# Kernel optimization log

Measured on AMD Instinct MI355X. Metric: run time of the kernel, lower is better.

Reference implementation:

```python
import jax, jax.numpy as jnp
import numpy as np

P = 50000    # number of POIs (rows of HG_pu, size of square A)
U = 100000   # number of users (rows of HG_up)
NNZ = 1600000
D = 128      # emb_dim


def setup_inputs() -> dict:
    key = jax.random.key(0)
    ks = jax.random.split(key, 8)
    x = jax.random.normal(ks[0], (P, D), dtype=jnp.float32)
    e = jax.random.normal(ks[1], (P, D), dtype=jnp.float32)
    vals_up = jax.random.uniform(ks[2], (NNZ,), dtype=jnp.float32)
    vals_pu = jax.random.uniform(ks[3], (NNZ,), dtype=jnp.float32)
    rows_up = jax.random.randint(ks[4], (NNZ,), 0, U, dtype=jnp.int32)
    cols_up = jax.random.randint(ks[5], (NNZ,), 0, P, dtype=jnp.int32)
    rows_pu = jax.random.randint(ks[6], (NNZ,), 0, P, dtype=jnp.int32)
    cols_pu = jax.random.randint(ks[7], (NNZ,), 0, U, dtype=jnp.int32)
    return {"t": 0, "x": x, "e": e,
            "vals_up": vals_up, "vals_pu": vals_pu,
            "rows_up": rows_up, "cols_up": cols_up,
            "rows_pu": rows_pu, "cols_pu": cols_pu}


def _spmm(vals, rows, cols, dense, num_rows):
    # sparse [num_rows, *] @ dense -> [num_rows, D]
    gathered = vals[:, None] * dense[cols]          # [nnz, D]
    return jax.ops.segment_sum(gathered, rows, num_segments=num_rows)


def reference(t, x, e, vals_up, vals_pu, rows_up, cols_up, rows_pu, cols_pu):
    # A = HG_pu @ HG_up (never materialized);  out = (A - I) @ x + e
    y = _spmm(vals_up, rows_up, cols_up, x, U)      # HG_up @ x : [U, D]
    z = _spmm(vals_pu, rows_pu, cols_pu, y, P)      # HG_pu @ y : [P, D]
    return z - x + e                                # (A - I) x + e
```

## Files before the change

kernel.cpp:

```cpp
#include <hip/hip_runtime.h>

#define NP 50000
#define NU 100000
#define NNZ_C 1600000
#define NNZ2 (2 * NNZ_C)
#define DIM 128
#define NR_TOT (NU + NP)

#define RBSH 7
#define RB 128
#define NBK ((NR_TOT + RB - 1) / RB)
#define ITEMS 8192
#define IPT (ITEMS / 256)
#define NBLK ((NNZ2 + ITEMS - 1) / ITEMS)

__device__ inline unsigned pack_bf16x2(float a, float b) {
    unsigned ia = __float_as_uint(a), ib = __float_as_uint(b);
    ia = (ia + 0x7FFFu + ((ia >> 16) & 1u)) >> 16;
    ib = (ib + 0x7FFFu + ((ib >> 16) & 1u)) >> 16;
    return ia | (ib << 16);
}

__device__ inline float dec_val(unsigned p) {
    return __uint_as_float((p & 0x7FFFu) << 16);
}

__global__ void cvt_bf16_kernel(const float* __restrict__ x,
                                unsigned* __restrict__ xh, int nwords) {
    int i = blockIdx.x * blockDim.x + threadIdx.x;
    if (i >= nwords) return;
    float2 v = ((const float2*)x)[i];
    xh[i] = pack_bf16x2(v.x, v.y);
}


__global__ void p1_hist_kernel(const int* __restrict__ rows_up,
                               const int* __restrict__ rows_pu,
                               int* __restrict__ hist_all) {
    __shared__ int h[NBK];
    for (int k = threadIdx.x; k < NBK; k += 256) h[k] = 0;
    __syncthreads();
    int base = blockIdx.x * ITEMS;
    for (int k = 0; k < IPT; ++k) {
        int i = base + k * 256 + threadIdx.x;
        if (i >= NNZ2) break;
        int r = (i < NNZ_C) ? rows_up[i] : (NU + rows_pu[i - NNZ_C]);
        atomicAdd(&h[r >> RBSH], 1);
    }
    __syncthreads();
    for (int k = threadIdx.x; k < NBK; k += 256)
        hist_all[k * NBLK + blockIdx.x] = h[k];
}

__global__ void p1_scan_kernel(const int* __restrict__ hist_all,
                               int* __restrict__ base_all,
                               int* __restrict__ totals) {
    __shared__ int lds[512];
    int b = blockIdx.x;
    int v = (threadIdx.x < NBLK) ? hist_all[b * NBLK + threadIdx.x] : 0;
    lds[threadIdx.x] = v;
    __syncthreads();
    for (int off = 1; off < 512; off <<= 1) {
        int t = (threadIdx.x >= (unsigned)off) ? lds[threadIdx.x - off] : 0;
        __syncthreads();
        lds[threadIdx.x] += t;
        __syncthreads();
    }
    if (threadIdx.x < NBLK) base_all[b * NBLK + threadIdx.x] = lds[threadIdx.x] - v;
    if (threadIdx.x == 511) totals[b] = lds[511];
}

__global__ void bucket_base_scan_kernel(const int* __restrict__ totals,
                                        int* __restrict__ bbase) {
    __shared__ int lds[1024];
    __shared__ int carry;
    if (threadIdx.x == 0) carry = 0;
    __syncthreads();
    for (int start = 0; start < NBK; start += 1024) {
        int i = start + threadIdx.x;
        int v = (i < NBK) ? totals[i] : 0;
        lds[threadIdx.x] = v;
        __syncthreads();
        for (int off = 1; off < 1024; off <<= 1) {
            int t = (threadIdx.x >= (unsigned)off) ? lds[threadIdx.x - off] : 0;
            __syncthreads();
            lds[threadIdx.x] += t;
            __syncthreads();
        }
        if (i < NBK) bbase[i] = carry + lds[threadIdx.x] - v;
        int tot = lds[1023];
        __syncthreads();
        if (threadIdx.x == 0) carry += tot;
        __syncthreads();
    }
    if (threadIdx.x == 0) bbase[NBK] = carry;
}

__global__ void p1_scatter_kernel(const float* __restrict__ vals_up,
                                  const float* __restrict__ vals_pu,
                                  const int* __restrict__ rows_up,
                                  const int* __restrict__ rows_pu,
                                  const int* __restrict__ cols_up,
                                  const int* __restrict__ cols_pu,
                                  const int* __restrict__ base_all,
                                  const int* __restrict__ bbase,
                                  int2* __restrict__ staging) {
    __shared__ int off[NBK];
    for (int k = threadIdx.x; k < NBK; k += 256) off[k] = 0;
    __syncthreads();
    int base = blockIdx.x * ITEMS;
    for (int k = 0; k < IPT; ++k) {
        int i = base + k * 256 + threadIdx.x;
        if (i >= NNZ2) break;
        int r, c; float v;
        if (i < NNZ_C) { r = rows_up[i]; c = cols_up[i]; v = vals_up[i]; }
        else { int q = i - NNZ_C; r = NU + rows_pu[q]; c = cols_pu[q]; v = vals_pu[q]; }
        int b = r >> RBSH;
        int lp = atomicAdd(&off[b], 1);
        unsigned vb = __float_as_uint(v);
        unsigned vr = (vb + 0x7FFFu + ((vb >> 16) & 1u)) >> 16;
        int pos = bbase[b] + base_all[b * NBLK + blockIdx.x] + lp;
        staging[pos] = make_int2((int)(((unsigned)c << 15) | vr), r);
    }
}

__global__ void p2_finalize_kernel(const int2* __restrict__ staging,
                                   const int* __restrict__ bbase,
                                   unsigned* __restrict__ packed,
                                   int* __restrict__ row_beg,
                                   int* __restrict__ row_cnt) {
    __shared__ int cnt[RB];
    __shared__ int scn[RB];
    __shared__ int cur[RB];
    int b = blockIdx.x;
    int beg = bbase[b], end = bbase[b + 1];
    if (threadIdx.x < RB) cnt[threadIdx.x] = 0;
    __syncthreads();
    for (int i = beg + threadIdx.x; i < end; i += 256)
        atomicAdd(&cnt[staging[i].y & (RB - 1)], 1);
    __syncthreads();
    if (threadIdx.x < RB) scn[threadIdx.x] = cnt[threadIdx.x];
    __syncthreads();
    for (int off = 1; off < RB; off <<= 1) {
        int t = 0;
        if (threadIdx.x < RB && threadIdx.x >= (unsigned)off) t = scn[threadIdx.x - off];
        __syncthreads();
        if (threadIdx.x < RB) scn[threadIdx.x] += t;
        __syncthreads();
    }
    if (threadIdx.x < RB) {
        int excl = scn[threadIdx.x] - cnt[threadIdx.x];
        cur[threadIdx.x] = beg + excl;
        int rr = (b << RBSH) + threadIdx.x;
        if (rr < NR_TOT) { row_beg[rr] = beg + excl; row_cnt[rr] = cnt[threadIdx.x]; }
    }
    __syncthreads();
    for (int i = beg + threadIdx.x; i < end; i += 256) {
        int2 it = staging[i];
        int pos = atomicAdd(&cur[it.y & (RB - 1)], 1);
        packed[pos] = (unsigned)it.x;
    }
}


__device__ inline void gather_row(const unsigned* __restrict__ packed,
                                  const unsigned* __restrict__ src,
                                  int beg, int end, int lane, float2& acc) {
    for (int chunk = beg; chunk < end; chunk += 64) {
        int cn = min(64, end - chunk);
        unsigned pw = (chunk + lane < end) ? packed[chunk + lane] : 0;
        int j = 0;
        for (; j + 7 < cn; j += 8) {
            unsigned p0 = (unsigned)__shfl((int)pw, j);
            unsigned p1 = (unsigned)__shfl((int)pw, j + 1);
            unsigned p2 = (unsigned)__shfl((int)pw, j + 2);
            unsigned p3 = (unsigned)__shfl((int)pw, j + 3);
            unsigned p4 = (unsigned)__shfl((int)pw, j + 4);
            unsigned p5 = (unsigned)__shfl((int)pw, j + 5);
            unsigned p6 = (unsigned)__shfl((int)pw, j + 6);
            unsigned p7 = (unsigned)__shfl((int)pw, j + 7);
            unsigned u0 = src[(p0 >> 15) * 64 + lane];
            unsigned u1 = src[(p1 >> 15) * 64 + lane];
            unsigned u2 = src[(p2 >> 15) * 64 + lane];
            unsigned u3 = src[(p3 >> 15) * 64 + lane];
            unsigned u4 = src[(p4 >> 15) * 64 + lane];
            unsigned u5 = src[(p5 >> 15) * 64 + lane];
            unsigned u6 = src[(p6 >> 15) * 64 + lane];
            unsigned u7 = src[(p7 >> 15) * 64 + lane];
            acc.x += dec_val(p0) * __uint_as_float(u0 << 16);
            acc.y += dec_val(p0) * __uint_as_float(u0 & 0xFFFF0000u);
            acc.x += dec_val(p1) * __uint_as_float(u1 << 16);
            acc.y += dec_val(p1) * __uint_as_float(u1 & 0xFFFF0000u);
            acc.x += dec_val(p2) * __uint_as_float(u2 << 16);
            acc.y += dec_val(p2) * __uint_as_float(u2 & 0xFFFF0000u);
            acc.x += dec_val(p3) * __uint_as_float(u3 << 16);
            acc.y += dec_val(p3) * __uint_as_float(u3 & 0xFFFF0000u);
            acc.x += dec_val(p4) * __uint_as_float(u4 << 16);
            acc.y += dec_val(p4) * __uint_as_float(u4 & 0xFFFF0000u);
            acc.x += dec_val(p5) * __uint_as_float(u5 << 16);
            acc.y += dec_val(p5) * __uint_as_float(u5 & 0xFFFF0000u);
            acc.x += dec_val(p6) * __uint_as_float(u6 << 16);
            acc.y += dec_val(p6) * __uint_as_float(u6 & 0xFFFF0000u);
            acc.x += dec_val(p7) * __uint_as_float(u7 << 16);
            acc.y += dec_val(p7) * __uint_as_float(u7 & 0xFFFF0000u);
        }
        for (; j + 3 < cn; j += 4) {
            unsigned p0 = (unsigned)__shfl((int)pw, j);
            unsigned p1 = (unsigned)__shfl((int)pw, j + 1);
            unsigned p2 = (unsigned)__shfl((int)pw, j + 2);
            unsigned p3 = (unsigned)__shfl((int)pw, j + 3);
            unsigned u0 = src[(p0 >> 15) * 64 + lane];
            unsigned u1 = src[(p1 >> 15) * 64 + lane];
            unsigned u2 = src[(p2 >> 15) * 64 + lane];
            unsigned u3 = src[(p3 >> 15) * 64 + lane];
            acc.x += dec_val(p0) * __uint_as_float(u0 << 16);
            acc.y += dec_val(p0) * __uint_as_float(u0 & 0xFFFF0000u);
            acc.x += dec_val(p1) * __uint_as_float(u1 << 16);
            acc.y += dec_val(p1) * __uint_as_float(u1 & 0xFFFF0000u);
            acc.x += dec_val(p2) * __uint_as_float(u2 << 16);
            acc.y += dec_val(p2) * __uint_as_float(u2 & 0xFFFF0000u);
            acc.x += dec_val(p3) * __uint_as_float(u3 << 16);
            acc.y += dec_val(p3) * __uint_as_float(u3 & 0xFFFF0000u);
        }
        for (; j < cn; ++j) {
            unsigned p = (unsigned)__shfl((int)pw, j);
            unsigned u = src[(p >> 15) * 64 + lane];
            float v = dec_val(p);
            acc.x += v * __uint_as_float(u << 16);
            acc.y += v * __uint_as_float(u & 0xFFFF0000u);
        }
    }
}

__global__ void spmm_gather_kernel(const int* __restrict__ row_beg,
                                   const int* __restrict__ row_cnt,
                                   const unsigned* __restrict__ packed,
                                   const unsigned* __restrict__ src,
                                   unsigned* __restrict__ dst) {
    int r = blockIdx.x * 4 + (threadIdx.x >> 6);
    if (r >= NU) return;
    int lane = threadIdx.x & 63;
    int beg = row_beg[r], end = beg + row_cnt[r];
    float2 acc = make_float2(0.f, 0.f);
    gather_row(packed, src, beg, end, lane, acc);
    dst[r * 64 + lane] = pack_bf16x2(acc.x, acc.y);
}

__global__ void spmm_gather_fused_kernel(const int* __restrict__ row_beg,
                                         const int* __restrict__ row_cnt,
                                         const unsigned* __restrict__ packed,
                                         const unsigned* __restrict__ src,
                                         const float* __restrict__ x,
                                         const float* __restrict__ e,
                                         float* __restrict__ out) {
    int r = blockIdx.x * 4 + (threadIdx.x >> 6);
    if (r >= NP) return;
    int lane = threadIdx.x & 63;
    int beg = row_beg[NU + r], end = beg + row_cnt[NU + r];
    float2 acc = make_float2(0.f, 0.f);
    gather_row(packed, src, beg, end, lane, acc);
    float2 xv = ((const float2*)(x + (size_t)r * DIM))[lane];
    float2 ev = ((const float2*)(e + (size_t)r * DIM))[lane];
    float2 o;
    o.x = acc.x - xv.x + ev.x;
    o.y = acc.y - xv.y + ev.y;
    ((float2*)(out + (size_t)r * DIM))[lane] = o;
}

extern "C" void kernel_launch(void* const* d_in, const int* in_sizes, int n_in,
                              void* d_out, int out_size, void* d_ws, size_t ws_size,
                              hipStream_t stream) {
    const float* x       = (const float*)d_in[1];
    const float* e       = (const float*)d_in[2];
    const float* vals_up = (const float*)d_in[3];
    const float* vals_pu = (const float*)d_in[4];
    const int*   rows_up = (const int*)d_in[5];
    const int*   cols_up = (const int*)d_in[6];
    const int*   rows_pu = (const int*)d_in[7];
    const int*   cols_pu = (const int*)d_in[8];
    float* out = (float*)d_out;

    char* ws = (char*)d_ws;
    unsigned* yh     = (unsigned*)(ws);
    int2* staging    = (int2*)(ws);
    unsigned* xh     = (unsigned*)(ws + 25600000);
    unsigned* packed = (unsigned*)(ws + 38400000);
    int* hist_all    = (int*)(ws + 51200000);
    int* base_all    = (int*)(ws + 53033248);
    int* totals      = (int*)(ws + 54866496);
    int* bbase       = (int*)(ws + 54871184);
    int* row_beg     = (int*)(ws + 54875904);
    int* row_cnt     = (int*)(ws + 55475904);

    cvt_bf16_kernel<<<(NP * 64 + 255) / 256, 256, 0, stream>>>(x, xh, NP * 64);

    p1_hist_kernel<<<NBLK, 256, 0, stream>>>(rows_up, rows_pu, hist_all);
    p1_scan_kernel<<<NBK, 512, 0, stream>>>(hist_all, base_all, totals);
    bucket_base_scan_kernel<<<1, 1024, 0, stream>>>(totals, bbase);
    p1_scatter_kernel<<<NBLK, 256, 0, stream>>>(vals_up, vals_pu,
                                                rows_up, rows_pu,
                                                cols_up, cols_pu,
                                                base_all, bbase, staging);
    p2_finalize_kernel<<<NBK, 256, 0, stream>>>(staging, bbase, packed,
                                                row_beg, row_cnt);

    spmm_gather_kernel<<<(NU + 3) / 4, 256, 0, stream>>>(row_beg, row_cnt,
                                                         packed, xh, yh);

    spmm_gather_fused_kernel<<<(NP + 3) / 4, 256, 0, stream>>>(row_beg, row_cnt,
                                                               packed, yh,
                                                               x, e, out);
}
```

Measured before the change: 387.3 us.

## Locally sort scatter chunks in LDS and split staging into payload and row byte

The bucket scatter kernel now processes each block's items in chunks of 4096. It builds a per-chunk bucket histogram and scan in shared memory, reorders entries by bucket in LDS, and then writes them to global staging in contiguous runs, so the scattered global stores become more coalesced. Staging is also split into a 4-byte payload array and a 1-byte local-row array instead of an 8-byte int2, which cuts staging traffic in both the scatter and finalize kernels. The cost is extra shared memory, more barriers and scan work per chunk, and lower occupancy from the larger LDS footprint.

Result: faster. 349.0 us (-9.9%).

```diff
diff --git a/kernel.cpp b/kernel.cpp
--- a/kernel.cpp
+++ b/kernel.cpp
@@ -11,8 +11,9 @@
 #define RB 128
 #define NBK ((NR_TOT + RB - 1) / RB)
 #define ITEMS 8192
-#define IPT (ITEMS / 256)
 #define NBLK ((NNZ2 + ITEMS - 1) / ITEMS)
+#define CHUNK 4096
+#define CPT (CHUNK / 256)
 
 __device__ inline unsigned pack_bf16x2(float a, float b) {
     unsigned ia = __float_as_uint(a), ib = __float_as_uint(b);
@@ -41,7 +42,7 @@
     for (int k = threadIdx.x; k < NBK; k += 256) h[k] = 0;
     __syncthreads();
     int base = blockIdx.x * ITEMS;
-    for (int k = 0; k < IPT; ++k) {
+    for (int k = 0; k < ITEMS / 256; ++k) {
         int i = base + k * 256 + threadIdx.x;
         if (i >= NNZ2) break;
         int r = (i < NNZ_C) ? rows_up[i] : (NU + rows_pu[i - NNZ_C]);
@@ -104,27 +105,92 @@
                                   const int* __restrict__ cols_pu,
                                   const int* __restrict__ base_all,
                                   const int* __restrict__ bbase,
-                                  int2* __restrict__ staging) {
+                                  unsigned* __restrict__ stag_pay,
+                                  unsigned char* __restrict__ stag_row) {
+    __shared__ unsigned spay[CHUNK];
+    __shared__ unsigned char srow[CHUNK];
+    __shared__ int sdst[CHUNK];
+    __shared__ int h[NBK];
+    __shared__ int cbase[NBK];
     __shared__ int off[NBK];
-    for (int k = threadIdx.x; k < NBK; k += 256) off[k] = 0;
-    __syncthreads();
-    int base = blockIdx.x * ITEMS;
-    for (int k = 0; k < IPT; ++k) {
-        int i = base + k * 256 + threadIdx.x;
-        if (i >= NNZ2) break;
-        int r, c; float v;
-        if (i < NNZ_C) { r = rows_up[i]; c = cols_up[i]; v = vals_up[i]; }
-        else { int q = i - NNZ_C; r = NU + rows_pu[q]; c = cols_pu[q]; v = vals_pu[q]; }
-        int b = r >> RBSH;
-        int lp = atomicAdd(&off[b], 1);
-        unsigned vb = __float_as_uint(v);
-        unsigned vr = (vb + 0x7FFFu + ((vb >> 16) & 1u)) >> 16;
-        int pos = bbase[b] + base_all[b * NBLK + blockIdx.x] + lp;
-        staging[pos] = make_int2((int)(((unsigned)c << 15) | vr), r);
-    }
-}
-
-__global__ void p2_finalize_kernel(const int2* __restrict__ staging,
+    __shared__ int tsum[256];
+
+    int tid = threadIdx.x;
+    int blk = blockIdx.x;
+    for (int k = tid; k < NBK; k += 256)
+        cbase[k] = bbase[k] + base_all[k * NBLK + blk];
+    int base = blk * ITEMS;
+
+    for (int c = 0; c < ITEMS / CHUNK; ++c) {
+        int cbeg = base + c * CHUNK;
+        int cnt_items = NNZ2 - cbeg;
+        if (cnt_items <= 0) break;
+        if (cnt_items > CHUNK) cnt_items = CHUNK;
+
+        for (int k = tid; k < NBK; k += 256) { h[k] = 0; off[k] = 0; }
+        __syncthreads();
+
+        unsigned rpay[CPT];
+        int rrow[CPT];
+        for (int k = 0; k < CPT; ++k) {
+            int i = cbeg + k * 256 + tid;
+            if (i < NNZ2) {
+                int r, cc; float v;
+                if (i < NNZ_C) { r = rows_up[i]; cc = cols_up[i]; v = vals_up[i]; }
+                else { int q = i - NNZ_C; r = NU + rows_pu[q]; cc = cols_pu[q]; v = vals_pu[q]; }
+                unsigned vb = __float_as_uint(v);
+                unsigned vr = (vb + 0x7FFFu + ((vb >> 16) & 1u)) >> 16;
+                rpay[k] = ((unsigned)cc << 15) | vr;
+                rrow[k] = r;
+                atomicAdd(&h[r >> RBSH], 1);
+            } else {
+                rrow[k] = -1;
+            }
+        }
+        __syncthreads();
+
+        {
+            int s0 = tid * 5;
+            int s1 = s0 + 5; if (s1 > NBK) s1 = NBK; if (s0 > NBK) s0 = NBK;
+            int a = 0;
+            for (int s = s0; s < s1; ++s) a += h[s];
+            tsum[tid] = a;
+            __syncthreads();
+            for (int o = 1; o < 256; o <<= 1) {
+                int t2 = (tid >= o) ? tsum[tid - o] : 0;
+                __syncthreads();
+                tsum[tid] += t2;
+                __syncthreads();
+            }
+            int run = (tid == 0) ? 0 : tsum[tid - 1];
+            for (int s = s0; s < s1; ++s) { int cc2 = h[s]; h[s] = run; run += cc2; }
+        }
+        __syncthreads();
+
+        for (int k = 0; k < CPT; ++k) {
+            if (rrow[k] < 0) continue;
+            int b = rrow[k] >> RBSH;
+            int lp = atomicAdd(&off[b], 1);
+            int slot = h[b] + lp;
+            spay[slot] = rpay[k];
+            srow[slot] = (unsigned char)(rrow[k] & (RB - 1));
+            sdst[slot] = cbase[b] + lp;
+        }
+        __syncthreads();
+
+        for (int s = tid; s < cnt_items; s += 256) {
+            int d = sdst[s];
+            stag_pay[d] = spay[s];
+            stag_row[d] = srow[s];
+        }
+        __syncthreads();
+        for (int k = tid; k < NBK; k += 256) cbase[k] += off[k];
+        __syncthreads();
+    }
+}
+
+__global__ void p2_finalize_kernel(const unsigned* __restrict__ stag_pay,
+                                   const unsigned char* __restrict__ stag_row,
                                    const int* __restrict__ bbase,
                                    unsigned* __restrict__ packed,
                                    int* __restrict__ row_beg,
@@ -137,7 +203,7 @@
     if (threadIdx.x < RB) cnt[threadIdx.x] = 0;
     __syncthreads();
     for (int i = beg + threadIdx.x; i < end; i += 256)
-        atomicAdd(&cnt[staging[i].y & (RB - 1)], 1);
+        atomicAdd(&cnt[stag_row[i]], 1);
     __syncthreads();
     if (threadIdx.x < RB) scn[threadIdx.x] = cnt[threadIdx.x];
     __syncthreads();
@@ -156,9 +222,8 @@
     }
     __syncthreads();
     for (int i = beg + threadIdx.x; i < end; i += 256) {
-        int2 it = staging[i];
-        int pos = atomicAdd(&cur[it.y & (RB - 1)], 1);
-        packed[pos] = (unsigned)it.x;
+        int pos = atomicAdd(&cur[stag_row[i]], 1);
+        packed[pos] = stag_pay[i];
     }
 }
 
@@ -281,8 +346,9 @@
     float* out = (float*)d_out;
 
     char* ws = (char*)d_ws;
-    unsigned* yh     = (unsigned*)(ws);
-    int2* staging    = (int2*)(ws);
+    unsigned* yh          = (unsigned*)(ws);
+    unsigned* stag_pay    = (unsigned*)(ws);
+    unsigned char* stag_row = (unsigned char*)(ws + 12800000);
     unsigned* xh     = (unsigned*)(ws + 25600000);
     unsigned* packed = (unsigned*)(ws + 38400000);
     int* hist_all    = (int*)(ws + 51200000);
@@ -300,9 +366,10 @@
     p1_scatter_kernel<<<NBLK, 256, 0, stream>>>(vals_up, vals_pu,
                                                 rows_up, rows_pu,
                                                 cols_up, cols_pu,
-                                                base_all, bbase, staging);
-    p2_finalize_kernel<<<NBK, 256, 0, stream>>>(staging, bbase, packed,
-                                                row_beg, row_cnt);
+                                                base_all, bbase,
+                                                stag_pay, stag_row);
+    p2_finalize_kernel<<<NBK, 256, 0, stream>>>(stag_pay, stag_row, bbase,
+                                                packed, row_beg, row_cnt);
 
     spmm_gather_kernel<<<(NU + 3) / 4, 256, 0, stream>>>(row_beg, row_cnt,
                                                          packed, xh, yh);
```
